# Kernel optimization log

Measured on AMD Instinct MI355X. Metric: run time of the kernel, lower is better.

The kernel has to match this reference:

```python
import jax, jax.numpy as jnp
import numpy as np
from jax import lax

B, M, N = 4096, 306, 984
LAMBDA = 0.1
MAX_ITER = 50


def setup_inputs() -> dict:
    key = jax.random.key(0)
    k1, k2, k3, k4 = jax.random.split(key, 4)
    return {
        "r_real": jax.random.normal(k1, (B, M), dtype=jnp.float32),
        "r_imag": jax.random.normal(k2, (B, M), dtype=jnp.float32),
        # phi buffer: torch.randn(M, N, dtype=complex64) -> real/imag each ~N(0, 1/2)?
        # torch.randn(complex64) draws real & imag each from N(0, 1/sqrt(2)^2)=N(0,0.5).
        "phi_real": jax.random.normal(k3, (M, N), dtype=jnp.float32) * np.float32(1.0 / np.sqrt(2.0)),
        "phi_imag": jax.random.normal(k4, (M, N), dtype=jnp.float32) * np.float32(1.0 / np.sqrt(2.0)),
    }


def reference(r_real, r_imag, phi_real, phi_imag):
    phi = (phi_real + 1j * phi_imag).astype(jnp.complex64)          # [M, N]
    r = (r_real + 1j * r_imag).astype(jnp.complex64)                # [B, M]
    # step_size = 1 / ||phi||_2^2  (spectral norm squared)
    step = (1.0 / jnp.linalg.norm(phi, ord=2) ** 2).real.astype(jnp.float32)
    thresh = (LAMBDA * step).astype(jnp.float32)
    phi_c = jnp.conj(phi)

    def body(w, _):
        # error = w @ phi.T - r : [B, M]
        error = jnp.einsum("bn,mn->bm", w, phi) - r
        # gradient = error @ conj(phi) : [B, N]
        grad = jnp.einsum("bm,mn->bn", error, phi_c)
        w_next = w - step * grad
        w_mag = jnp.abs(w_next)
        new_mag = jax.nn.relu(w_mag - thresh)
        # polar(new_mag, angle(w_next))
        w_new = (new_mag * jnp.exp(1j * jnp.angle(w_next))).astype(jnp.complex64)
        return w_new, None

    w0 = jnp.zeros((r.shape[0], N), dtype=jnp.complex64)
    w, _ = lax.scan(body, w0, None, length=MAX_ITER)
    return jnp.abs(w).astype(jnp.float32)
```

## Files before the change

### kernel.cpp

```cpp
#include <hip/hip_runtime.h>
#include <math.h>

#define Bb 4096
#define Mm 306
#define Nn 984
#define NCP 1024
#define KA 2048
#define ITERS 50
#define KSQ 9

typedef _Float16 f16x8 __attribute__((ext_vector_type(8)));
typedef float f32x16 __attribute__((ext_vector_type(16)));

__device__ __forceinline__ void cmac(float2& c, const float2 a, const float2 b) {
    c.x = fmaf(a.x, b.x, c.x);
    c.x = fmaf(-a.y, b.y, c.x);
    c.y = fmaf(a.x, b.y, c.y);
    c.y = fmaf(a.y, b.x, c.y);
}

__device__ __forceinline__ unsigned short f16bits(float v) {
    union { _Float16 h; unsigned short u; } cv;
    cv.h = (_Float16)v;
    return cv.u;
}
__device__ __forceinline__ float f16lo(unsigned int u) {
    union { unsigned short s; _Float16 h; } cv; cv.s = (unsigned short)(u & 0xffffu);
    return (float)cv.h;
}
__device__ __forceinline__ float f16hi(unsigned int u) {
    union { unsigned short s; _Float16 h; } cv; cv.s = (unsigned short)(u >> 16);
    return (float)cv.h;
}

__device__ __forceinline__ void load_lds16(const void* g, void* l) {
    __builtin_amdgcn_global_load_lds((const __attribute__((address_space(1))) void*)g,
                                     (__attribute__((address_space(3))) void*)l, 16, 0, 0);
}

__device__ __forceinline__ size_t swzA(int b, int c) {
    return ((size_t)(((b >> 7) * 32 + (c >> 5)) * 1024 + ((c >> 2) & 7) * 128 + (b & 127))) * 4 + (c & 3);
}
__device__ __forceinline__ size_t swzB(int jr, int q) {
    return ((size_t)(((jr >> 7) * 32 + (q >> 5)) * 1024 + ((q >> 2) & 7) * 128 + (jr & 127))) * 4 + (q & 3);
}
__device__ __forceinline__ size_t swzA2(int b, int c) {
    return ((size_t)(((b >> 7) * 10 + (c >> 5)) * 1024 + ((c >> 2) & 7) * 128 + (b & 127))) * 4 + (c & 3);
}
__device__ __forceinline__ size_t swzB2(int jr, int q) {
    return ((size_t)(((jr >> 7) * 10 + (q >> 5)) * 1024 + ((q >> 2) & 7) * 128 + (jr & 127))) * 4 + (q & 3);
}

__global__ void gram_kernel(const float* __restrict__ pr, const float* __restrict__ pi,
                            float2* __restrict__ G) {
    __shared__ float2 As[32][33];
    __shared__ float2 Bs[32][33];
    int tx = threadIdx.x, ty = threadIdx.y;
    int t = ty * 16 + tx;
    int i0 = blockIdx.y * 32, j0 = blockIdx.x * 32;
    int zs = blockIdx.z * 246;
    int ze = zs + 246 < Nn ? zs + 246 : Nn;
    float2 acc[2][2] = {};
    for (int k0 = zs; k0 < ze; k0 += 32) {
        #pragma unroll
        for (int rep = 0; rep < 4; ++rep) {
            int idx = t + rep * 256;
            int rr = idx >> 5, cc = idx & 31;
            int gk = k0 + cc;
            int gi = i0 + rr, gj = j0 + rr;
            float2 a = make_float2(0.f, 0.f), b = make_float2(0.f, 0.f);
            if (gk < ze) {
                if (gi < Mm) a = make_float2(pr[(size_t)gi * Nn + gk], pi[(size_t)gi * Nn + gk]);
                if (gj < Mm) b = make_float2(pr[(size_t)gj * Nn + gk], pi[(size_t)gj * Nn + gk]);
            }
            As[rr][cc] = a; Bs[rr][cc] = b;
        }
        __syncthreads();
        #pragma unroll 8
        for (int kk = 0; kk < 32; ++kk) {
            float2 a0 = As[ty * 2][kk], a1 = As[ty * 2 + 1][kk];
            float2 b0 = Bs[tx * 2][kk], b1 = Bs[tx * 2 + 1][kk];
            #define GMAC(qq, aa, bb) \
                qq.x = fmaf(aa.x, bb.x, qq.x); qq.x = fmaf(aa.y, bb.y, qq.x); \
                qq.y = fmaf(aa.y, bb.x, qq.y); qq.y = fmaf(-aa.x, bb.y, qq.y);
            GMAC(acc[0][0], a0, b0) GMAC(acc[0][1], a0, b1)
            GMAC(acc[1][0], a1, b0) GMAC(acc[1][1], a1, b1)
            #undef GMAC
        }
        __syncthreads();
    }
    #pragma unroll
    for (int i = 0; i < 2; ++i) {
        int gi = i0 + ty * 2 + i;
        #pragma unroll
        for (int j = 0; j < 2; ++j) {
            int gj = j0 + tx * 2 + j;
            if (gi < Mm && gj < Mm) {
                atomicAdd(&G[gi * Mm + gj].x, acc[i][j].x);
                atomicAdd(&G[gi * Mm + gj].y, acc[i][j].y);
            }
        }
    }
}

__global__ void frob_kernel(const float2* __restrict__ H, float* __restrict__ slot, int n) {
    int idx = blockIdx.x * blockDim.x + threadIdx.x;
    int stride = gridDim.x * blockDim.x;
    float s = 0.f;
    for (int i = idx; i < n; i += stride) {
        float2 v = H[i];
        s = fmaf(v.x, v.x, s);
        s = fmaf(v.y, v.y, s);
    }
    #pragma unroll
    for (int o = 32; o > 0; o >>= 1) s += __shfl_down(s, o, 64);
    __shared__ float wsum[4];
    int lane = threadIdx.x & 63, wv = threadIdx.x >> 6;
    if (lane == 0) wsum[wv] = s;
    __syncthreads();
    if (threadIdx.x == 0) atomicAdd(slot, wsum[0] + wsum[1] + wsum[2] + wsum[3]);
}

__global__ void sqmm_kernel(const float2* __restrict__ A, float2* __restrict__ C,
                            const float* __restrict__ fslot) {
    __shared__ float2 As[32][33];
    __shared__ float2 Bs[32][33];
    float inv = 1.0f / fslot[0];
    int tx = threadIdx.x, ty = threadIdx.y;
    int t = ty * 16 + tx;
    int r0 = blockIdx.y * 32, c0 = blockIdx.x * 32;
    int zs = blockIdx.z * 80;
    int ze = zs + 80 < Mm ? zs + 80 : Mm;
    float2 acc[2][2] = {};
    for (int k0 = zs; k0 < ze; k0 += 32) {
        #pragma unroll
        for (int i = 0; i < 4; ++i) {
            int idx = t + i * 256;
            int rr = idx >> 5, cc = idx & 31;
            int gr = r0 + rr, gk = k0 + cc;
            As[rr][cc] = (gr < Mm && gk < ze) ? A[gr * Mm + gk] : make_float2(0.f, 0.f);
            int gk2 = k0 + rr, gc = c0 + cc;
            Bs[rr][cc] = (gk2 < ze && gc < Mm) ? A[gk2 * Mm + gc] : make_float2(0.f, 0.f);
        }
        __syncthreads();
        #pragma unroll 8
        for (int kk = 0; kk < 32; ++kk) {
            float2 a0 = As[ty * 2][kk], a1 = As[ty * 2 + 1][kk];
            float2 b0 = Bs[kk][tx * 2], b1 = Bs[kk][tx * 2 + 1];
            cmac(acc[0][0], a0, b0); cmac(acc[0][1], a0, b1);
            cmac(acc[1][0], a1, b0); cmac(acc[1][1], a1, b1);
        }
        __syncthreads();
    }
    #pragma unroll
    for (int i = 0; i < 2; ++i) {
        int gr = r0 + ty * 2 + i;
        #pragma unroll
        for (int j = 0; j < 2; ++j) {
            int gc = c0 + tx * 2 + j;
            if (gr < Mm && gc < Mm) {
                atomicAdd(&C[gr * Mm + gc].x, acc[i][j].x * inv);
                atomicAdd(&C[gr * Mm + gc].y, acc[i][j].y * inv);
            }
        }
    }
}

__global__ void rayleigh_kernel(const float2* __restrict__ H, const float2* __restrict__ G,
                                float* __restrict__ sc) {
    __shared__ float2 v[Mm];
    __shared__ float rn[320], rd[320];
    int t = threadIdx.x;
    if (t < Mm) {
        float2 s = make_float2(0.f, 0.f);
        for (int j = 0; j < Mm; ++j) { float2 h = H[t * Mm + j]; s.x += h.x; s.y += h.y; }
        v[t] = s;
    }
    __syncthreads();
    float num = 0.f, den = 0.f;
    if (t < Mm) {
        float2 u = make_float2(0.f, 0.f);
        for (int k = 0; k < Mm; ++k) {
            float2 g = G[k * Mm + t];
            float2 vk = v[k];
            u.x = fmaf(g.x, vk.x, u.x); u.x = fmaf(g.y, vk.y, u.x);
            u.y = fmaf(g.x, vk.y, u.y); u.y = fmaf(-g.y, vk.x, u.y);
        }
        float2 vt = v[t];
        num = vt.x * u.x + vt.y * u.y;
        den = vt.x * vt.x + vt.y * vt.y;
    }
    rn[t] = num; rd[t] = den;
    __syncthreads();
    if (t == 0) {
        float sn = 0.f, sd = 0.f;
        for (int i = 0; i < 320; ++i) { sn += rn[i]; sd += rd[i]; }
        float lam = sn / sd;
        float step = 1.0f / lam;
        sc[0] = step;
        sc[1] = 0.1f * step;
    }
}

__global__ void qpack_kernel(const float* __restrict__ pr, const float* __restrict__ pi,
                             unsigned int* __restrict__ Bu, const float* __restrict__ sc) {
    __shared__ float2 Pn[16][33];
    __shared__ float2 Pc[16][33];
    float nstep = -sc[0];
    int t = threadIdx.x;
    int tx = t & 15, ty = t >> 4;
    int n0 = blockIdx.x * 32, c0 = blockIdx.y * 32;
    float2 q[2][2] = {};
    for (int m0 = 0; m0 < Mm; m0 += 16) {
        #pragma unroll
        for (int rep = 0; rep < 2; ++rep) {
            int idx = t + rep * 256;
            int mm = idx >> 5, col = idx & 31;
            int gm = m0 + mm;
            float2 a = make_float2(0.f, 0.f), b = make_float2(0.f, 0.f);
            if (gm < Mm) {
                if (n0 + col < Nn) a = make_float2(pr[(size_t)gm * Nn + n0 + col], pi[(size_t)gm * Nn + n0 + col]);
                if (c0 + col < Nn) b = make_float2(pr[(size_t)gm * Nn + c0 + col], pi[(size_t)gm * Nn + c0 + col]);
            }
            Pn[mm][col] = a; Pc[mm][col] = b;
        }
        __syncthreads();
        #pragma unroll
        for (int mm = 0; mm < 16; ++mm) {
            float2 a0 = Pn[mm][ty * 2], a1 = Pn[mm][ty * 2 + 1];
            float2 b0 = Pc[mm][tx * 2], b1 = Pc[mm][tx * 2 + 1];
            #define QMAC(qq, aa, bb) \
                qq.x = fmaf(aa.x, bb.x, qq.x); qq.x = fmaf(aa.y, bb.y, qq.x); \
                qq.y = fmaf(aa.y, bb.x, qq.y); qq.y = fmaf(-aa.x, bb.y, qq.y);
            QMAC(q[0][0], a0, b0) QMAC(q[0][1], a0, b1)
            QMAC(q[1][0], a1, b0) QMAC(q[1][1], a1, b1)
            #undef QMAC
        }
        __syncthreads();
    }
    #pragma unroll
    for (int i = 0; i < 2; ++i) {
        int n = n0 + ty * 2 + i;
        #pragma unroll
        for (int j = 0; j < 2; ++j) {
            int c = c0 + tx * 2 + j;
            if (n < Nn && c < Nn) {
                float MR = nstep * q[i][j].x, MI = nstep * q[i][j].y;
                unsigned short hR = f16bits(MR);
                unsigned short hI = f16bits(MI);
                unsigned short nhI = hI ^ 0x8000u;
                int jr = ((c >> 5) * 64) + (c & 31);
                Bu[swzB(jr, n)]      = (unsigned)hR | ((unsigned)nhI << 16);
                Bu[swzB(jr + 32, n)] = (unsigned)hI | ((unsigned)hR << 16);
            }
        }
    }
}

__global__ void rpack_kernel(const float* __restrict__ rr, const float* __restrict__ ri,
                             unsigned int* __restrict__ rp16) {
    int b = blockIdx.x * 256 + threadIdx.x;
    int m = blockIdx.y;
    rp16[swzA2(b, m)] = (unsigned)f16bits(rr[(size_t)b * Mm + m]) |
                        ((unsigned)f16bits(ri[(size_t)b * Mm + m]) << 16);
}

__global__ void ppack2_kernel(const float* __restrict__ pr, const float* __restrict__ pi,
                              unsigned int* __restrict__ B2u, const float* __restrict__ sc) {
    int n = blockIdx.x * 256 + threadIdx.x;
    int m = blockIdx.y;
    if (n >= Nn) return;
    float s = sc[0];
    float xr = pr[(size_t)m * Nn + n], xi = pi[(size_t)m * Nn + n];
    unsigned short x = f16bits(-s * xr), y = f16bits(-s * xi);
    int jr2 = ((n >> 5) * 64) + (n & 31);
    B2u[swzB2(jr2, m)]      = (unsigned)x | ((unsigned)y << 16);
    B2u[swzB2(jr2 + 32, m)] = (unsigned)(y ^ 0x8000u) | ((unsigned)x << 16);
}

__global__ __launch_bounds__(256, 2) void rphi_mfma_kernel(
    const _Float16* __restrict__ rp16, const _Float16* __restrict__ B2,
    unsigned int* __restrict__ rph16) {
    __shared__ _Float16 As[2][8192];
    __shared__ _Float16 Bs[2][8192];
    int tid = threadIdx.x;
    int lane = tid & 63, wv = tid >> 6;
    int wm = wv & 1, wn = wv >> 1;
    int bblk = blockIdx.x, nblk = blockIdx.y;
    int l31 = lane & 31, lh = lane >> 5;

    f32x16 acc[2][2] = {};

    const char* gabase = (const char*)rp16 + ((size_t)bblk * 10 * 1024) * 16;
    const char* gbbase = (const char*)B2 + ((size_t)nblk * 10 * 1024) * 16;

    #pragma unroll
    for (int c = 0; c < 4; ++c) {
        int u = c * 256 + tid;
        load_lds16(gabase + (size_t)u * 16, &As[0][(size_t)(c * 256 + wv * 64) * 8]);
        load_lds16(gbbase + (size_t)u * 16, &Bs[0][(size_t)(c * 256 + wv * 64) * 8]);
    }
    __syncthreads();

    for (int kt = 0; kt < 10; ++kt) {
        int cur = kt & 1;
        if (kt + 1 < 10) {
            #pragma unroll
            for (int c = 0; c < 4; ++c) {
                int u = c * 256 + tid;
                load_lds16(gabase + ((size_t)(kt + 1) * 1024 + u) * 16,
                           &As[cur ^ 1][(size_t)(c * 256 + wv * 64) * 8]);
                load_lds16(gbbase + ((size_t)(kt + 1) * 1024 + u) * 16,
                           &Bs[cur ^ 1][(size_t)(c * 256 + wv * 64) * 8]);
            }
        }
        #pragma unroll
        for (int s = 0; s < 4; ++s) {
            int kq = s * 2 + lh;
            f16x8 af[2], bfr[2];
            #pragma unroll
            for (int mt = 0; mt < 2; ++mt)
                af[mt] = *reinterpret_cast<const f16x8*>(
                    &As[cur][(size_t)(kq * 128 + wm * 64 + mt * 32 + l31) * 8]);
            #pragma unroll
            for (int nt = 0; nt < 2; ++nt)
                bfr[nt] = *reinterpret_cast<const f16x8*>(
                    &Bs[cur][(size_t)(kq * 128 + wn * 64 + nt * 32 + l31) * 8]);
            #pragma unroll
            for (int mt = 0; mt < 2; ++mt)
                #pragma unroll
                for (int nt = 0; nt < 2; ++nt)
                    acc[mt][nt] = __builtin_amdgcn_mfma_f32_32x32x16_f16(af[mt], bfr[nt], acc[mt][nt], 0, 0, 0);
        }
        __syncthreads();
    }

    int b0 = bblk * 128;
    int c = nblk * 64 + wn * 32 + l31;
    #pragma unroll
    for (int mt = 0; mt < 2; ++mt) {
        #pragma unroll
        for (int reg = 0; reg < 16; ++reg) {
            int row = b0 + wm * 64 + mt * 32 + ((reg & 3) + 8 * (reg >> 2) + 4 * lh);
            rph16[(size_t)row * NCP + c] =
                (unsigned)f16bits(-acc[mt][0][reg]) | ((unsigned)f16bits(-acc[mt][1][reg]) << 16);
        }
    }
}

__global__ __launch_bounds__(256, 2) void ista7_kernel(
    const _Float16* __restrict__ wfi, const _Float16* __restrict__ Bq,
    unsigned int* __restrict__ wfo,
    const unsigned int* __restrict__ rph16,
    const float* __restrict__ sc, float* __restrict__ out, int last) {
    __shared__ _Float16 As[2][8192];
    __shared__ _Float16 Bs[2][8192];
    int tid = threadIdx.x;
    int lane = tid & 63, wv = tid >> 6;
    int wm = wv & 1, wn = wv >> 1;
    int id = blockIdx.x;
    int bblk = id >> 4;
    int nblk = id & 15;
    int l31 = lane & 31, lh = lane >> 5;

    f32x16 acc[2][2] = {};

    const char* gabase = (const char*)wfi + ((size_t)bblk * 32 * 1024) * 16;
    const char* gbbase = (const char*)Bq + ((size_t)nblk * 32 * 1024) * 16;

    #pragma unroll
    for (int c = 0; c < 4; ++c) {
        int u = c * 256 + tid;
        load_lds16(gabase + (size_t)u * 16, &As[0][(size_t)(c * 256 + wv * 64) * 8]);
        load_lds16(gbbase + (size_t)u * 16, &Bs[0][(size_t)(c * 256 + wv * 64) * 8]);
    }
    __syncthreads();

    for (int kt = 0; kt < 32; ++kt) {
        int cur = kt & 1;
        if (kt + 1 < 32) {
            #pragma unroll
            for (int c = 0; c < 4; ++c) {
                int u = c * 256 + tid;
                load_lds16(gabase + ((size_t)(kt + 1) * 1024 + u) * 16,
                           &As[cur ^ 1][(size_t)(c * 256 + wv * 64) * 8]);
                load_lds16(gbbase + ((size_t)(kt + 1) * 1024 + u) * 16,
                           &Bs[cur ^ 1][(size_t)(c * 256 + wv * 64) * 8]);
            }
        }
        #pragma unroll
        for (int s = 0; s < 4; ++s) {
            int kq = s * 2 + lh;
            f16x8 af[2], bfr[2];
            #pragma unroll
            for (int mt = 0; mt < 2; ++mt)
                af[mt] = *reinterpret_cast<const f16x8*>(
                    &As[cur][(size_t)(kq * 128 + wm * 64 + mt * 32 + l31) * 8]);
            #pragma unroll
            for (int nt = 0; nt < 2; ++nt)
                bfr[nt] = *reinterpret_cast<const f16x8*>(
                    &Bs[cur][(size_t)(kq * 128 + wn * 64 + nt * 32 + l31) * 8]);
            #pragma unroll
            for (int mt = 0; mt < 2; ++mt)
                #pragma unroll
                for (int nt = 0; nt < 2; ++nt)
                    acc[mt][nt] = __builtin_amdgcn_mfma_f32_32x32x16_f16(af[mt], bfr[nt], acc[mt][nt], 0, 0, 0);
        }
        __syncthreads();
    }

    float thr = sc[1];
    int b0 = bblk * 128;
    int c = nblk * 64 + wn * 32 + l31;
    const unsigned int* wfin = (const unsigned int*)wfi;
    #pragma unroll
    for (int mt = 0; mt < 2; ++mt) {
        #pragma unroll
        for (int reg = 0; reg < 16; ++reg) {
            int row = b0 + wm * 64 + mt * 32 + ((reg & 3) + 8 * (reg >> 2) + 4 * lh);
            unsigned int wu = wfin[swzA(row, c)];
            unsigned int ru = rph16[(size_t)row * NCP + c];
            float zr = f16lo(wu) + acc[mt][0][reg] + f16lo(ru);
            float zi = f16hi(wu) + acc[mt][1][reg] + f16hi(ru);
            float mag = sqrtf(zr * zr + zi * zi);
            float nm = mag - thr;
            float f = (nm > 0.f) ? (nm / mag) : 0.f;
            wfo[swzA(row, c)] = (unsigned)f16bits(zr * f) | ((unsigned)f16bits(zi * f) << 16);
            if (last && c < Nn) out[(size_t)row * Nn + c] = fmaxf(nm, 0.f);
        }
    }
}

extern "C" void kernel_launch(void* const* d_in, const int* in_sizes, int n_in,
                              void* d_out, int out_size, void* d_ws, size_t ws_size,
                              hipStream_t stream) {
    const float* rr = (const float*)d_in[0];
    const float* ri = (const float*)d_in[1];
    const float* pr = (const float*)d_in[2];
    const float* pi = (const float*)d_in[3];
    float* out = (float*)d_out;

    char* ws = (char*)d_ws;
    size_t off = 0;
    _Float16* wf0 = (_Float16*)(ws + off); off += (size_t)Bb * KA * sizeof(_Float16);
    _Float16* wf1 = (_Float16*)(ws + off); off += (size_t)Bb * KA * sizeof(_Float16);
    _Float16* Bq  = (_Float16*)(ws + off); off += (size_t)2048 * 2048 * sizeof(_Float16);
    unsigned int* rph16 = (unsigned int*)(ws + off); off += (size_t)Bb * NCP * 4;
    _Float16* rp16 = (_Float16*)(ws + off); off += (size_t)Bb * 640 * sizeof(_Float16);
    _Float16* B2  = (_Float16*)(ws + off); off += (size_t)2048 * 640 * sizeof(_Float16);
    float2* G = (float2*)(ws + off);     off += (size_t)Mm * Mm * sizeof(float2);
    float2* H1 = (float2*)(ws + off);    off += (size_t)Mm * Mm * sizeof(float2);
    float2* H2 = (float2*)(ws + off);    off += (size_t)Mm * Mm * sizeof(float2);
    float* slots = (float*)(ws + off);   off += 64 * sizeof(float);
    float* sc = slots + 32;

    (void)hipMemsetAsync(wf0, 0, (size_t)Bb * KA * sizeof(_Float16), stream);
    (void)hipMemsetAsync(Bq, 0, (size_t)2048 * 2048 * sizeof(_Float16), stream);
    (void)hipMemsetAsync(rp16, 0, (size_t)Bb * 640 * sizeof(_Float16), stream);
    (void)hipMemsetAsync(B2, 0, (size_t)2048 * 640 * sizeof(_Float16), stream);
    (void)hipMemsetAsync(slots, 0, 64 * sizeof(float), stream);
    (void)hipMemsetAsync(G, 0, (size_t)Mm * Mm * sizeof(float2), stream);

    gram_kernel<<<dim3(10, 10, 4), dim3(16, 16), 0, stream>>>(pr, pi, G);
    float2* bufs[2] = { H1, H2 };
    const float2* src = G;
    for (int s = 0; s < KSQ; ++s) {
        frob_kernel<<<128, 256, 0, stream>>>(src, slots + s, Mm * Mm);
        float2* dst = bufs[s & 1];
        (void)hipMemsetAsync(dst, 0, (size_t)Mm * Mm * sizeof(float2), stream);
        sqmm_kernel<<<dim3(10, 10, 4), dim3(16, 16), 0, stream>>>(src, dst, slots + s);
        src = dst;
    }
    rayleigh_kernel<<<1, 320, 0, stream>>>(src, G, sc);

    qpack_kernel<<<dim3(31, 31), 256, 0, stream>>>(pr, pi, (unsigned int*)Bq, sc);
    rpack_kernel<<<dim3(16, Mm), 256, 0, stream>>>(rr, ri, (unsigned int*)rp16);
    ppack2_kernel<<<dim3(4, Mm), 256, 0, stream>>>(pr, pi, (unsigned int*)B2, sc);
    rphi_mfma_kernel<<<dim3(32, 16), 256, 0, stream>>>(rp16, B2, rph16);

    _Float16* wbuf[2] = { wf0, wf1 };
    for (int it = 0; it < ITERS; ++it) {
        ista7_kernel<<<512, 256, 0, stream>>>(
            wbuf[it & 1], Bq, (unsigned int*)wbuf[(it + 1) & 1], rph16, sc, out,
            it == ITERS - 1 ? 1 : 0);
    }
}
```

Before: 3.183 ms.

## Fold identity into Gram matrix and drop LDS double buffering

The qpack kernel now adds the identity to the diagonal of the -step*Phi^H Phi matrix, so the ISTA GEMM produces w + step-update directly. This removes the per-element reload of the previous w in the epilogue. Both MFMA kernels drop their double-buffered LDS staging for a single buffer, loaded and synchronized at each k-step, which halves LDS use and may allow higher occupancy but loses load/compute overlap. The qpack shared tiles are also split into separate real and imaginary arrays. Holding 1+small values in fp16 loses precision on the diagonal term.

```diff
diff --git a/kernel.cpp b/kernel.cpp
--- a/kernel.cpp
+++ b/kernel.cpp
@@ -204,8 +204,8 @@
 
 __global__ void qpack_kernel(const float* __restrict__ pr, const float* __restrict__ pi,
                              unsigned int* __restrict__ Bu, const float* __restrict__ sc) {
-    __shared__ float2 Pn[16][33];
-    __shared__ float2 Pc[16][33];
+    __shared__ float Pnr[16][33], Pni[16][33];
+    __shared__ float Pcr[16][33], Pci[16][33];
     float nstep = -sc[0];
     int t = threadIdx.x;
     int tx = t & 15, ty = t >> 4;
@@ -222,13 +222,16 @@
                 if (n0 + col < Nn) a = make_float2(pr[(size_t)gm * Nn + n0 + col], pi[(size_t)gm * Nn + n0 + col]);
                 if (c0 + col < Nn) b = make_float2(pr[(size_t)gm * Nn + c0 + col], pi[(size_t)gm * Nn + c0 + col]);
             }
-            Pn[mm][col] = a; Pc[mm][col] = b;
+            Pnr[mm][col] = a.x; Pni[mm][col] = a.y;
+            Pcr[mm][col] = b.x; Pci[mm][col] = b.y;
         }
         __syncthreads();
         #pragma unroll
         for (int mm = 0; mm < 16; ++mm) {
-            float2 a0 = Pn[mm][ty * 2], a1 = Pn[mm][ty * 2 + 1];
-            float2 b0 = Pc[mm][tx * 2], b1 = Pc[mm][tx * 2 + 1];
+            float2 a0 = make_float2(Pnr[mm][ty * 2], Pni[mm][ty * 2]);
+            float2 a1 = make_float2(Pnr[mm][ty * 2 + 1], Pni[mm][ty * 2 + 1]);
+            float2 b0 = make_float2(Pcr[mm][tx * 2], Pci[mm][tx * 2]);
+            float2 b1 = make_float2(Pcr[mm][tx * 2 + 1], Pci[mm][tx * 2 + 1]);
             #define QMAC(qq, aa, bb) \
                 qq.x = fmaf(aa.x, bb.x, qq.x); qq.x = fmaf(aa.y, bb.y, qq.x); \
                 qq.y = fmaf(aa.y, bb.x, qq.y); qq.y = fmaf(-aa.x, bb.y, qq.y);
@@ -245,7 +248,8 @@
         for (int j = 0; j < 2; ++j) {
             int c = c0 + tx * 2 + j;
             if (n < Nn && c < Nn) {
-                float MR = nstep * q[i][j].x, MI = nstep * q[i][j].y;
+                float MR = fmaf(nstep, q[i][j].x, (n == c) ? 1.0f : 0.0f);
+                float MI = nstep * q[i][j].y;
                 unsigned short hR = f16bits(MR);
                 unsigned short hI = f16bits(MI);
                 unsigned short nhI = hI ^ 0x8000u;
@@ -281,8 +285,8 @@
 __global__ __launch_bounds__(256, 2) void rphi_mfma_kernel(
     const _Float16* __restrict__ rp16, const _Float16* __restrict__ B2,
     unsigned int* __restrict__ rph16) {
-    __shared__ _Float16 As[2][8192];
-    __shared__ _Float16 Bs[2][8192];
+    __shared__ _Float16 As[8192];
+    __shared__ _Float16 Bs[8192];
     int tid = threadIdx.x;
     int lane = tid & 63, wv = tid >> 6;
     int wm = wv & 1, wn = wv >> 1;
@@ -291,29 +295,16 @@
 
     f32x16 acc[2][2] = {};
 
-    const char* gabase = (const char*)rp16 + ((size_t)bblk * 10 * 1024) * 16;
-    const char* gbbase = (const char*)B2 + ((size_t)nblk * 10 * 1024) * 16;
-
-    #pragma unroll
-    for (int c = 0; c < 4; ++c) {
-        int u = c * 256 + tid;
-        load_lds16(gabase + (size_t)u * 16, &As[0][(size_t)(c * 256 + wv * 64) * 8]);
-        load_lds16(gbbase + (size_t)u * 16, &Bs[0][(size_t)(c * 256 + wv * 64) * 8]);
-    }
-    __syncthreads();
-
     for (int kt = 0; kt < 10; ++kt) {
-        int cur = kt & 1;
-        if (kt + 1 < 10) {
-            #pragma unroll
-            for (int c = 0; c < 4; ++c) {
-                int u = c * 256 + tid;
-                load_lds16(gabase + ((size_t)(kt + 1) * 1024 + u) * 16,
-                           &As[cur ^ 1][(size_t)(c * 256 + wv * 64) * 8]);
-                load_lds16(gbbase + ((size_t)(kt + 1) * 1024 + u) * 16,
-                           &Bs[cur ^ 1][(size_t)(c * 256 + wv * 64) * 8]);
-            }
-        }
+        #pragma unroll
+        for (int c = 0; c < 4; ++c) {
+            int u = c * 256 + tid;
+            const char* ga = (const char*)rp16 + (((size_t)(bblk * 10 + kt)) * 1024 + u) * 16;
+            load_lds16(ga, &As[(size_t)(c * 256 + wv * 64) * 8]);
+            const char* gb = (const char*)B2 + (((size_t)(nblk * 10 + kt)) * 1024 + u) * 16;
+            load_lds16(gb, &Bs[(size_t)(c * 256 + wv * 64) * 8]);
+        }
+        __syncthreads();
         #pragma unroll
         for (int s = 0; s < 4; ++s) {
             int kq = s * 2 + lh;
@@ -321,11 +312,11 @@
             #pragma unroll
             for (int mt = 0; mt < 2; ++mt)
                 af[mt] = *reinterpret_cast<const f16x8*>(
-                    &As[cur][(size_t)(kq * 128 + wm * 64 + mt * 32 + l31) * 8]);
+                    &As[(size_t)(kq * 128 + wm * 64 + mt * 32 + l31) * 8]);
             #pragma unroll
             for (int nt = 0; nt < 2; ++nt)
                 bfr[nt] = *reinterpret_cast<const f16x8*>(
-                    &Bs[cur][(size_t)(kq * 128 + wn * 64 + nt * 32 + l31) * 8]);
+                    &Bs[(size_t)(kq * 128 + wn * 64 + nt * 32 + l31) * 8]);
             #pragma unroll
             for (int mt = 0; mt < 2; ++mt)
                 #pragma unroll
@@ -353,8 +344,8 @@
     unsigned int* __restrict__ wfo,
     const unsigned int* __restrict__ rph16,
     const float* __restrict__ sc, float* __restrict__ out, int last) {
-    __shared__ _Float16 As[2][8192];
-    __shared__ _Float16 Bs[2][8192];
+    __shared__ _Float16 As[8192];
+    __shared__ _Float16 Bs[8192];
     int tid = threadIdx.x;
     int lane = tid & 63, wv = tid >> 6;
     int wm = wv & 1, wn = wv >> 1;
@@ -365,29 +356,16 @@
 
     f32x16 acc[2][2] = {};
 
-    const char* gabase = (const char*)wfi + ((size_t)bblk * 32 * 1024) * 16;
-    const char* gbbase = (const char*)Bq + ((size_t)nblk * 32 * 1024) * 16;
-
-    #pragma unroll
-    for (int c = 0; c < 4; ++c) {
-        int u = c * 256 + tid;
-        load_lds16(gabase + (size_t)u * 16, &As[0][(size_t)(c * 256 + wv * 64) * 8]);
-        load_lds16(gbbase + (size_t)u * 16, &Bs[0][(size_t)(c * 256 + wv * 64) * 8]);
-    }
-    __syncthreads();
-
     for (int kt = 0; kt < 32; ++kt) {
-        int cur = kt & 1;
-        if (kt + 1 < 32) {
-            #pragma unroll
-            for (int c = 0; c < 4; ++c) {
-                int u = c * 256 + tid;
-                load_lds16(gabase + ((size_t)(kt + 1) * 1024 + u) * 16,
-                           &As[cur ^ 1][(size_t)(c * 256 + wv * 64) * 8]);
-                load_lds16(gbbase + ((size_t)(kt + 1) * 1024 + u) * 16,
-                           &Bs[cur ^ 1][(size_t)(c * 256 + wv * 64) * 8]);
-            }
-        }
+        #pragma unroll
+        for (int c = 0; c < 4; ++c) {
+            int u = c * 256 + tid;
+            const char* ga = (const char*)wfi + (((size_t)(bblk * 32 + kt)) * 1024 + u) * 16;
+            load_lds16(ga, &As[(size_t)(c * 256 + wv * 64) * 8]);
+            const char* gb = (const char*)Bq + (((size_t)(nblk * 32 + kt)) * 1024 + u) * 16;
+            load_lds16(gb, &Bs[(size_t)(c * 256 + wv * 64) * 8]);
+        }
+        __syncthreads();
         #pragma unroll
         for (int s = 0; s < 4; ++s) {
             int kq = s * 2 + lh;
@@ -395,11 +373,11 @@
             #pragma unroll
             for (int mt = 0; mt < 2; ++mt)
                 af[mt] = *reinterpret_cast<const f16x8*>(
-                    &As[cur][(size_t)(kq * 128 + wm * 64 + mt * 32 + l31) * 8]);
+                    &As[(size_t)(kq * 128 + wm * 64 + mt * 32 + l31) * 8]);
             #pragma unroll
             for (int nt = 0; nt < 2; ++nt)
                 bfr[nt] = *reinterpret_cast<const f16x8*>(
-                    &Bs[cur][(size_t)(kq * 128 + wn * 64 + nt * 32 + l31) * 8]);
+                    &Bs[(size_t)(kq * 128 + wn * 64 + nt * 32 + l31) * 8]);
             #pragma unroll
             for (int mt = 0; mt < 2; ++mt)
                 #pragma unroll
@@ -412,16 +390,14 @@
     float thr = sc[1];
     int b0 = bblk * 128;
     int c = nblk * 64 + wn * 32 + l31;
-    const unsigned int* wfin = (const unsigned int*)wfi;
     #pragma unroll
     for (int mt = 0; mt < 2; ++mt) {
         #pragma unroll
         for (int reg = 0; reg < 16; ++reg) {
             int row = b0 + wm * 64 + mt * 32 + ((reg & 3) + 8 * (reg >> 2) + 4 * lh);
-            unsigned int wu = wfin[swzA(row, c)];
             unsigned int ru = rph16[(size_t)row * NCP + c];
-            float zr = f16lo(wu) + acc[mt][0][reg] + f16lo(ru);
-            float zi = f16hi(wu) + acc[mt][1][reg] + f16hi(ru);
+            float zr = acc[mt][0][reg] + f16lo(ru);
+            float zi = acc[mt][1][reg] + f16hi(ru);
             float mag = sqrtf(zr * zr + zi * zi);
             float nm = mag - thr;
             float f = (nm > 0.f) ? (nm / mag) : 0.f;
```

Measured after the change: 3.006 ms. 1.06x faster.
